# Kernel optimization log

Measured on AMD Instinct MI355X. Metric: run time of the kernel, lower is better.

Reference implementation:

```python
import jax, jax.numpy as jnp
import numpy as np
from jax.scipy.special import i0

# ---- NFFT configuration (matches init_kwargs) ----
N = (256, 256)          # output spectral size
n = (512, 512)          # oversampled grid size (sigma = 2)
M_PTS = 262144          # nonequispaced points
MWIN = 4                # window cutoff m
SIGMA = 2.0             # n[i]/N[i]
B_KB = (2.0 - 1.0 / SIGMA) * np.pi  # Kaiser-Bessel shape parameter

_n_arr = jnp.asarray(n, dtype=jnp.float32)


def _phi(k):
    """Kaiser-Bessel window, k: (..., d) -> (...,). Matches KaiserBesselWindow.forward."""
    arg = jnp.sqrt(MWIN ** 2 - (_n_arr * k) ** 2)
    out = jnp.sinh(B_KB * arg) / (arg * jnp.pi)
    out = jnp.nan_to_num(out, nan=0.0)
    return jnp.prod(out, axis=-1)


def _phi_hat():
    """Fourier coefficients of the window on the N-grid, shape (N1, N2)."""
    axes = [jnp.arange(-N[i] // 2, N[i] // 2, dtype=jnp.float32) for i in range(2)]
    grid = jnp.stack(jnp.meshgrid(*axes, indexing='ij'), axis=-1)  # (N1, N2, 2)
    ft = i0(MWIN * jnp.sqrt(B_KB ** 2 - (2.0 * jnp.pi * grid / _n_arr) ** 2))
    return jnp.prod(ft, axis=-1)


def setup_inputs() -> dict:
    key = jax.random.key(0)
    k1, k2, k3 = jax.random.split(key, 3)
    x = jax.random.uniform(k1, (1, 1, M_PTS, 2), dtype=jnp.float32,
                           minval=-0.5, maxval=0.5)
    f_hat_real = jax.random.normal(k2, (1, 1, N[0], N[1]), dtype=jnp.float32)
    f_hat_imag = jax.random.normal(k3, (1, 1, N[0], N[1]), dtype=jnp.float32)
    return {"x": x, "f_hat_real": f_hat_real, "f_hat_imag": f_hat_imag}


def _forward_nfft(x, f_hat):
    B, C = f_hat.shape[0], f_hat.shape[1]
    phi_hat = _phi_hat().astype(f_hat.real.dtype)
    # deconvolution + zero-padding to the oversampled grid
    g_hat = f_hat / phi_hat
    pad0 = (n[0] - N[0]) // 2
    pad1 = (n[1] - N[1]) // 2
    g_hat = jnp.pad(g_hat, ((0, 0), (0, 0), (pad0, pad0), (pad1, pad1)))
    # FFT (norm='backward': unnormalized forward transform)
    g_hat = jnp.fft.fftshift(g_hat, axes=(-2, -1))
    g = jnp.fft.fft2(g_hat)
    g = jnp.fft.ifftshift(g, axes=(-2, -1))  # (B, C, n1, n2)

    # ---- sparse (windowed) convolution: gather per point ----
    w = jnp.arange(2 * MWIN, dtype=jnp.int32)
    window = jnp.stack(jnp.meshgrid(w, w, indexing='ij'), axis=-1)
    window = window.reshape(-1, 1, 1, 1, 2)                    # (W,1,1,1,2)
    base = jnp.ceil(x * _n_arr).astype(jnp.int32) - MWIN        # (B,1,M,2)
    inds = base[None] + window                                  # (W,B,1,M,2)
    increments = _phi(x[None] - inds.astype(jnp.float32) / _n_arr)  # (W,B,1,M)
    n_i = jnp.asarray(n, dtype=jnp.int32)
    im = (inds + n_i // 2) % n_i                                # wrap to grid
    lin = im[..., 0] * n[1] + im[..., 1]                        # (W,B,1,M)
    lin = (lin
           + (n[0] * n[1]) * jnp.arange(C, dtype=jnp.int32).reshape(1, 1, C, 1)
           + (n[0] * n[1] * C) * jnp.arange(B, dtype=jnp.int32).reshape(1, B, 1, 1))
    g_l = g.reshape(-1)[lin]                                    # (W,B,C,M) gather
    f = jnp.sum(g_l * increments.astype(g.dtype), axis=0)       # (B,C,M)
    return f


def reference(x, f_hat_real, f_hat_imag):
    f_hat = (f_hat_real + 1j * f_hat_imag).astype(jnp.complex64)
    return _forward_nfft(x, f_hat)
```

## Files before the change

kernel.cpp:

```cpp
#include <hip/hip_runtime.h>
#include <math.h>

#define NPTS 262144
#define B_KB 4.71238898038469f
#define B_KB2 22.2066099025f
#define PI_F 3.14159265358979f
#define INV_2PI 0.15915494309f
#define TWO_PI_OVER_N 0.01227184630309f
#define NCOL 520
#define S_SCALE 1.37438953472e11f
#define INV_S   7.27595761418e-12f

typedef _Float16 half8v __attribute__((ext_vector_type(8)));
typedef _Float16 half4v __attribute__((ext_vector_type(4)));

__device__ __forceinline__ float i0f_dev(float x) {
    float ax = fabsf(x);
    if (ax < 3.75f) {
        float t = ax / 3.75f; t *= t;
        return 1.0f + t*(3.5156229f + t*(3.0899424f + t*(1.2067492f +
               t*(0.2659732f + t*(0.0360768f + t*0.0045813f)))));
    } else {
        float t = 3.75f / ax;
        float p = 0.39894228f + t*(0.01328592f + t*(0.00225319f + t*(-0.00157565f +
                  t*(0.00916281f + t*(-0.02057706f + t*(0.02635537f +
                  t*(-0.01647633f + t*0.00392377f)))))));
        return expf(ax) * p / sqrtf(ax);
    }
}

__device__ __forceinline__ float phi_win(float t) {
    float s = 16.0f - t * t;
    if (s <= 0.0f) return 0.0f;
    float a = sqrtf(s);
    float ez = __expf(B_KB * a);
    return (ez - __builtin_amdgcn_rcpf(ez)) * INV_2PI * __builtin_amdgcn_rcpf(a);
}

__global__ void rowfft_build(const float* __restrict__ fr,
                             const float* __restrict__ fi,
                             float2* __restrict__ g) {
    __shared__ float2 buf[512];
    int r = blockIdx.x;
    int i1 = (r < 128) ? r : r + 256;
    int k1 = (r < 128) ? r : r - 256;
    int tid = threadIdx.x;
    float a1 = TWO_PI_OVER_N * (float)k1;
    float ph1 = i0f_dev(4.0f * sqrtf(B_KB2 - a1 * a1));

    int k2 = tid - 128;
    int i2 = k2 & 511;
    float a2 = TWO_PI_OVER_N * (float)k2;
    float ph2 = i0f_dev(4.0f * sqrtf(B_KB2 - a2 * a2));
    float inv = S_SCALE / (ph1 * ph2);
    if ((i1 + i2) & 1) inv = -inv;
    int fidx = (k1 + 128) * 256 + (k2 + 128);
    float2 v = make_float2(fr[fidx] * inv, fi[fidx] * inv);

    buf[tid] = make_float2(0.0f, 0.0f);
    buf[tid + 256] = make_float2(0.0f, 0.0f);
    __syncthreads();
    int ri = (int)(__brev((unsigned)i2) >> 23);
    buf[ri] = v;
    __syncthreads();

    #pragma unroll
    for (int s = 1; s <= 9; ++s) {
        int half = 1 << (s - 1);
        int pos = tid & (half - 1);
        int j1 = ((tid >> (s - 1)) << s) | pos;
        float ang = -PI_F * (float)pos / (float)half;
        float sw, cw;
        __sincosf(ang, &sw, &cw);
        float2 u = buf[j1];
        float2 w = buf[j1 + half];
        float wr = cw * w.x - sw * w.y;
        float wi = cw * w.y + sw * w.x;
        buf[j1]        = make_float2(u.x + wr, u.y + wi);
        buf[j1 + half] = make_float2(u.x - wr, u.y - wi);
        __syncthreads();
    }
    long base = (long)i1 * NCOL;
    for (int j = tid; j < 512; j += 256) g[base + j] = buf[j];
    if (tid < 8) g[base + 512 + tid] = buf[tid];
}

__global__ void colfft_real(const float2* __restrict__ g,
                            float* __restrict__ gre) {
    __shared__ float2 buf[512];
    int c = blockIdx.x;
    int tid = threadIdx.x;
    buf[tid] = make_float2(0.0f, 0.0f);
    buf[tid + 256] = make_float2(0.0f, 0.0f);
    __syncthreads();
    int r = (tid < 128) ? tid : tid + 256;
    int rr = (int)(__brev((unsigned)r) >> 23);
    buf[rr] = g[(long)r * NCOL + c];
    __syncthreads();
    #pragma unroll
    for (int s = 1; s <= 9; ++s) {
        int half = 1 << (s - 1);
        int pos = tid & (half - 1);
        int j1 = ((tid >> (s - 1)) << s) | pos;
        float ang = -PI_F * (float)pos / (float)half;
        float sw, cw;
        __sincosf(ang, &sw, &cw);
        float2 u = buf[j1];
        float2 w = buf[j1 + half];
        float wr = cw * w.x - sw * w.y;
        float wi = cw * w.y + sw * w.x;
        buf[j1]        = make_float2(u.x + wr, u.y + wi);
        buf[j1 + half] = make_float2(u.x - wr, u.y - wi);
        __syncthreads();
    }
    for (int j = tid; j < 512; j += 256) gre[(long)j * NCOL + c] = buf[j].x;
}

__global__ void build_quads(const float* __restrict__ gre,
                            _Float16* __restrict__ qg) {
    int u = blockIdx.x;
    int s = u >> 7, rq = u & 127;
    int tid = threadIdx.x;
    int r0 = 4 * rq + s;
    const float* g0 = gre + (long)((r0    ) & 511) * NCOL;
    const float* g1 = gre + (long)((r0 + 1) & 511) * NCOL;
    const float* g2 = gre + (long)((r0 + 2) & 511) * NCOL;
    const float* g3 = gre + (long)((r0 + 3) & 511) * NCOL;
    _Float16* outb = qg + ((long)u * NCOL << 2);
    for (int c = tid; c < NCOL; c += 256) {
        half4v w;
        w[0] = (_Float16)g0[c];
        w[1] = (_Float16)g1[c];
        w[2] = (_Float16)g2[c];
        w[3] = (_Float16)g3[c];
        *reinterpret_cast<half4v*>(outb + ((long)c << 2)) = w;
    }
}

__global__ __launch_bounds__(256)
void gather_quads(const float2* __restrict__ x,
                  const _Float16* __restrict__ qg,
                  float* __restrict__ out) {
    int t = blockIdx.x * 256 + threadIdx.x;
    int m = t >> 1;
    int h = t & 1;
    float2 xv = x[m];
    float v1 = xv.x * 512.0f;
    float v2 = xv.y * 512.0f;
    float c1 = ceilf(v1), c2 = ceilf(v2);
    int b1 = (int)c1 - 4, b2 = (int)c2 - 4;
    float f1 = c1 - v1, f2 = c2 - v2;

    float phi2[8];
    #pragma unroll
    for (int j = 0; j < 8; ++j) phi2[j] = phi_win(4.0f - (float)j - f2);
    float phi1h[4];
    #pragma unroll
    for (int r = 0; r < 4; ++r)
        phi1h[r] = phi_win(4.0f - (float)(4 * h + r) - f1);

    int b1p = (b1 + 768) & 511;
    int b2p = (b2 + 768) & 511;
    int s  = b1p & 3;
    int rq = ((b1p >> 2) + h) & 127;
    const _Float16* base = qg + (((long)(s * 128 + rq) * NCOL + b2p) << 2);

    half8v rv[4];
    #pragma unroll
    for (int li = 0; li < 4; ++li)
        rv[li] = *reinterpret_cast<const half8v*>(base + (li << 3));

    float acc = 0.0f;
    #pragma unroll
    for (int li = 0; li < 4; ++li) {
        #pragma unroll
        for (int k = 0; k < 8; ++k) {
            int j = (li << 1) + (k >> 2);
            int r = k & 3;
            acc += (float)rv[li][k] * (phi1h[r] * phi2[j]);
        }
    }
    acc += __shfl_xor(acc, 1);
    if (h == 0) out[m] = acc * INV_S;
}

__global__ void build_ghat(const float* __restrict__ fr,
                           const float* __restrict__ fi,
                           float2* __restrict__ g, int ldg) {
    int idx = blockIdx.x * 256 + threadIdx.x;
    int i1 = idx >> 9;
    int i2 = idx & 511;
    float2 val = make_float2(0.0f, 0.0f);
    int k1 = 0, k2 = 0;
    bool ok = true;
    if (i1 < 128) k1 = i1; else if (i1 >= 384) k1 = i1 - 512; else ok = false;
    if (ok) { if (i2 < 128) k2 = i2; else if (i2 >= 384) k2 = i2 - 512; else ok = false; }
    if (ok) {
        float a1 = TWO_PI_OVER_N * (float)k1;
        float a2 = TWO_PI_OVER_N * (float)k2;
        float ph1 = i0f_dev(4.0f * sqrtf(B_KB2 - a1*a1));
        float ph2 = i0f_dev(4.0f * sqrtf(B_KB2 - a2*a2));
        float inv = 1.0f / (ph1 * ph2);
        if ((i1 + i2) & 1) inv = -inv;
        int fidx = (k1 + 128) * 256 + (k2 + 128);
        val.x = fr[fidx] * inv;
        val.y = fi[fidx] * inv;
    }
    g[i1 * ldg + i2] = val;
}

__global__ void fft_lines(float2* __restrict__ g, int line_stride,
                          int elem_stride, int ndup) {
    __shared__ float2 buf[512];
    int line = blockIdx.x;
    int tid = threadIdx.x;
    long base = (long)line * line_stride;
    for (int j = tid; j < 512; j += 256) {
        int rj = (int)(__brev((unsigned)j) >> 23);
        buf[rj] = g[base + (long)j * elem_stride];
    }
    __syncthreads();
    #pragma unroll
    for (int s = 1; s <= 9; ++s) {
        int half = 1 << (s - 1);
        int pos = tid & (half - 1);
        int i1 = ((tid >> (s - 1)) << s) | pos;
        float ang = -PI_F * (float)pos / (float)half;
        float sw, cw;
        __sincosf(ang, &sw, &cw);
        float2 u = buf[i1];
        float2 v = buf[i1 + half];
        float wr = cw * v.x - sw * v.y;
        float wi = cw * v.y + sw * v.x;
        buf[i1]        = make_float2(u.x + wr, u.y + wi);
        buf[i1 + half] = make_float2(u.x - wr, u.y - wi);
        __syncthreads();
    }
    for (int j = tid; j < 512; j += 256) g[base + (long)j * elem_stride] = buf[j];
    for (int j = tid; j < ndup; j += 256) g[base + 512 + j] = buf[j];
}

template<int COMPLEX>
__global__ __launch_bounds__(256, 4)
void gather_pad(const float2* __restrict__ x,
                const float2* __restrict__ g,
                float* __restrict__ out) {
    int m = blockIdx.x * 256 + threadIdx.x;
    float2 xv = x[m];
    float v1 = xv.x * 512.0f;
    float v2 = xv.y * 512.0f;
    float c1 = ceilf(v1), c2 = ceilf(v2);
    int b1 = (int)c1 - 4, b2 = (int)c2 - 4;
    float f1 = c1 - v1, f2 = c2 - v2;

    float phi1[8], phi2[8];
    int rowb[8];
    #pragma unroll
    for (int w = 0; w < 8; ++w) {
        phi1[w] = phi_win(4.0f - (float)w - f1);
        phi2[w] = phi_win(4.0f - (float)w - f2);
        rowb[w] = ((b1 + w + 768) & 511) * NCOL;
    }
    int cb = (b2 + 768) & 511;

    float accx = 0.0f, accy = 0.0f;
    #pragma unroll
    for (int w1 = 0; w1 < 8; ++w1) {
        const float4* p = reinterpret_cast<const float4*>(g + rowb[w1] + cb);
        float4 va = p[0], vb = p[1], vc = p[2], vd = p[3];
        float p1 = phi1[w1];
        accx += p1 * (phi2[0]*va.x + phi2[1]*va.z + phi2[2]*vb.x + phi2[3]*vb.z +
                      phi2[4]*vc.x + phi2[5]*vc.z + phi2[6]*vd.x + phi2[7]*vd.z);
        if (COMPLEX)
            accy += p1 * (phi2[0]*va.y + phi2[1]*va.w + phi2[2]*vb.y + phi2[3]*vb.w +
                          phi2[4]*vc.y + phi2[5]*vc.w + phi2[6]*vd.y + phi2[7]*vd.w);
    }
    if (COMPLEX) ((float2*)out)[m] = make_float2(accx, accy);
    else out[m] = accx;
}

extern "C" void kernel_launch(void* const* d_in, const int* in_sizes, int n_in,
                              void* d_out, int out_size, void* d_ws, size_t ws_size,
                              hipStream_t stream) {
    const float* x  = (const float*)d_in[0];
    const float* fr = (const float*)d_in[1];
    const float* fi = (const float*)d_in[2];
    int cplx = (out_size >= 2 * NPTS) ? 1 : 0;

    size_t g_bytes   = (size_t)512 * NCOL * sizeof(float2);
    size_t gre_bytes = (size_t)512 * NCOL * sizeof(float);
    size_t qg_bytes  = (size_t)512 * NCOL * 4 * sizeof(_Float16);
    char* ws = (char*)d_ws;
    float2*   g   = (float2*)ws;
    float*    gre = (float*)(ws + g_bytes);
    _Float16* qg  = (_Float16*)(ws + g_bytes + gre_bytes);
    size_t need = g_bytes + gre_bytes + qg_bytes;

    if (!cplx && ws_size >= need) {
        rowfft_build<<<256, 256, 0, stream>>>(fr, fi, g);
        colfft_real<<<NCOL, 256, 0, stream>>>(g, gre);
        build_quads<<<512, 256, 0, stream>>>(gre, qg);
        gather_quads<<<2048, 256, 0, stream>>>((const float2*)x, qg, (float*)d_out);
    } else if (ws_size >= g_bytes) {
        build_ghat<<<1024, 256, 0, stream>>>(fr, fi, g, NCOL);
        fft_lines<<<512, 256, 0, stream>>>(g, NCOL, 1, 8);
        fft_lines<<<NCOL, 256, 0, stream>>>(g, 1, NCOL, 0);
        if (cplx)
            gather_pad<1><<<1024, 256, 0, stream>>>((const float2*)x, g, (float*)d_out);
        else
            gather_pad<0><<<1024, 256, 0, stream>>>((const float2*)x, g, (float*)d_out);
    } else {
        build_ghat<<<1024, 256, 0, stream>>>(fr, fi, g, 512);
        fft_lines<<<512, 256, 0, stream>>>(g, 512, 1, 0);
        fft_lines<<<512, 256, 0, stream>>>(g, 1, 512, 0);
        if (cplx)
            gather_pad<1><<<1024, 256, 0, stream>>>((const float2*)x, g, (float*)d_out);
        else
            gather_pad<0><<<1024, 256, 0, stream>>>((const float2*)x, g, (float*)d_out);
    }
}
```

Before: 28.25 us.

## Pack eight grid rows per fp16 vector so each point reads one contiguous segment

```diff
diff --git a/kernel.cpp b/kernel.cpp
--- a/kernel.cpp
+++ b/kernel.cpp
@@ -12,7 +12,6 @@
 #define INV_S   7.27595761418e-12f
 
 typedef _Float16 half8v __attribute__((ext_vector_type(8)));
-typedef _Float16 half4v __attribute__((ext_vector_type(4)));
 
 __device__ __forceinline__ float i0f_dev(float x) {
     float ax = fabsf(x);
@@ -116,31 +115,35 @@
     for (int j = tid; j < 512; j += 256) gre[(long)j * NCOL + c] = buf[j].x;
 }
 
-__global__ void build_quads(const float* __restrict__ gre,
-                            _Float16* __restrict__ qg) {
+__global__ void build_octs(const float* __restrict__ gre,
+                           _Float16* __restrict__ og) {
     int u = blockIdx.x;
-    int s = u >> 7, rq = u & 127;
+    int s = u >> 6, ro = u & 63;
     int tid = threadIdx.x;
-    int r0 = 4 * rq + s;
-    const float* g0 = gre + (long)((r0    ) & 511) * NCOL;
-    const float* g1 = gre + (long)((r0 + 1) & 511) * NCOL;
-    const float* g2 = gre + (long)((r0 + 2) & 511) * NCOL;
-    const float* g3 = gre + (long)((r0 + 3) & 511) * NCOL;
-    _Float16* outb = qg + ((long)u * NCOL << 2);
+    int r0 = 8 * ro + s;
+    const float* gp0 = gre + (long)((r0    ) & 511) * NCOL;
+    const float* gp1 = gre + (long)((r0 + 1) & 511) * NCOL;
+    const float* gp2 = gre + (long)((r0 + 2) & 511) * NCOL;
+    const float* gp3 = gre + (long)((r0 + 3) & 511) * NCOL;
+    const float* gp4 = gre + (long)((r0 + 4) & 511) * NCOL;
+    const float* gp5 = gre + (long)((r0 + 5) & 511) * NCOL;
+    const float* gp6 = gre + (long)((r0 + 6) & 511) * NCOL;
+    const float* gp7 = gre + (long)((r0 + 7) & 511) * NCOL;
+    _Float16* outb = og + ((long)u * NCOL << 3);
     for (int c = tid; c < NCOL; c += 256) {
-        half4v w;
-        w[0] = (_Float16)g0[c];
-        w[1] = (_Float16)g1[c];
-        w[2] = (_Float16)g2[c];
-        w[3] = (_Float16)g3[c];
-        *reinterpret_cast<half4v*>(outb + ((long)c << 2)) = w;
+        half8v w;
+        w[0] = (_Float16)gp0[c]; w[1] = (_Float16)gp1[c];
+        w[2] = (_Float16)gp2[c]; w[3] = (_Float16)gp3[c];
+        w[4] = (_Float16)gp4[c]; w[5] = (_Float16)gp5[c];
+        w[6] = (_Float16)gp6[c]; w[7] = (_Float16)gp7[c];
+        *reinterpret_cast<half8v*>(outb + ((long)c << 3)) = w;
     }
 }
 
 __global__ __launch_bounds__(256)
-void gather_quads(const float2* __restrict__ x,
-                  const _Float16* __restrict__ qg,
-                  float* __restrict__ out) {
+void gather_oct(const float2* __restrict__ x,
+                const _Float16* __restrict__ og,
+                float* __restrict__ out) {
     int t = blockIdx.x * 256 + threadIdx.x;
     int m = t >> 1;
     int h = t & 1;
@@ -151,34 +154,28 @@
     int b1 = (int)c1 - 4, b2 = (int)c2 - 4;
     float f1 = c1 - v1, f2 = c2 - v2;
 
-    float phi2[8];
-    #pragma unroll
-    for (int j = 0; j < 8; ++j) phi2[j] = phi_win(4.0f - (float)j - f2);
-    float phi1h[4];
-    #pragma unroll
-    for (int r = 0; r < 4; ++r)
-        phi1h[r] = phi_win(4.0f - (float)(4 * h + r) - f1);
-
     int b1p = (b1 + 768) & 511;
     int b2p = (b2 + 768) & 511;
-    int s  = b1p & 3;
-    int rq = ((b1p >> 2) + h) & 127;
-    const _Float16* base = qg + (((long)(s * 128 + rq) * NCOL + b2p) << 2);
+    int s  = b1p & 7;
+    int ro = b1p >> 3;
+    const _Float16* seg = og + (((long)(s * 64 + ro) * NCOL + b2p) << 3);
 
     half8v rv[4];
     #pragma unroll
-    for (int li = 0; li < 4; ++li)
-        rv[li] = *reinterpret_cast<const half8v*>(base + (li << 3));
-
+    for (int i = 0; i < 4; ++i)
+        rv[i] = *reinterpret_cast<const half8v*>(seg + (((i << 1) | h) << 3));
+
+    float phi1[8];
+    #pragma unroll
+    for (int r = 0; r < 8; ++r) phi1[r] = phi_win(4.0f - (float)r - f1);
     float acc = 0.0f;
     #pragma unroll
-    for (int li = 0; li < 4; ++li) {
+    for (int i = 0; i < 4; ++i) {
+        float p2 = phi_win(4.0f - (float)((i << 1) | h) - f2);
+        float rs = 0.0f;
         #pragma unroll
-        for (int k = 0; k < 8; ++k) {
-            int j = (li << 1) + (k >> 2);
-            int r = k & 3;
-            acc += (float)rv[li][k] * (phi1h[r] * phi2[j]);
-        }
+        for (int r = 0; r < 8; ++r) rs += (float)rv[i][r] * phi1[r];
+        acc += p2 * rs;
     }
     acc += __shfl_xor(acc, 1);
     if (h == 0) out[m] = acc * INV_S;
@@ -289,18 +286,18 @@
 
     size_t g_bytes   = (size_t)512 * NCOL * sizeof(float2);
     size_t gre_bytes = (size_t)512 * NCOL * sizeof(float);
-    size_t qg_bytes  = (size_t)512 * NCOL * 4 * sizeof(_Float16);
+    size_t og_bytes  = (size_t)512 * NCOL * 8 * sizeof(_Float16);
     char* ws = (char*)d_ws;
     float2*   g   = (float2*)ws;
     float*    gre = (float*)(ws + g_bytes);
-    _Float16* qg  = (_Float16*)(ws + g_bytes + gre_bytes);
-    size_t need = g_bytes + gre_bytes + qg_bytes;
+    _Float16* og  = (_Float16*)(ws + g_bytes + gre_bytes);
+    size_t need = g_bytes + gre_bytes + og_bytes;
 
     if (!cplx && ws_size >= need) {
         rowfft_build<<<256, 256, 0, stream>>>(fr, fi, g);
         colfft_real<<<NCOL, 256, 0, stream>>>(g, gre);
-        build_quads<<<512, 256, 0, stream>>>(gre, qg);
-        gather_quads<<<2048, 256, 0, stream>>>((const float2*)x, qg, (float*)d_out);
+        build_octs<<<512, 256, 0, stream>>>(gre, og);
+        gather_oct<<<2048, 256, 0, stream>>>((const float2*)x, og, (float*)d_out);
     } else if (ws_size >= g_bytes) {
         build_ghat<<<1024, 256, 0, stream>>>(fr, fi, g, NCOL);
         fft_lines<<<512, 256, 0, stream>>>(g, NCOL, 1, 8);
```

Measured after the change: 30.99 us. 1.1x slower.

## Fuse column FFT with fp16 quad-grid build; split phi evaluation across lane pair

Applied to the files above, without the earlier changes.

```diff
diff --git a/kernel.cpp b/kernel.cpp
--- a/kernel.cpp
+++ b/kernel.cpp
@@ -85,8 +85,8 @@
     if (tid < 8) g[base + 512 + tid] = buf[tid];
 }
 
-__global__ void colfft_real(const float2* __restrict__ g,
-                            float* __restrict__ gre) {
+__global__ void colfft_quads(const float2* __restrict__ g,
+                             _Float16* __restrict__ qg) {
     __shared__ float2 buf[512];
     int c = blockIdx.x;
     int tid = threadIdx.x;
@@ -113,27 +113,18 @@
         buf[j1 + half] = make_float2(u.x - wr, u.y - wi);
         __syncthreads();
     }
-    for (int j = tid; j < 512; j += 256) gre[(long)j * NCOL + c] = buf[j].x;
-}
-
-__global__ void build_quads(const float* __restrict__ gre,
-                            _Float16* __restrict__ qg) {
-    int u = blockIdx.x;
-    int s = u >> 7, rq = u & 127;
-    int tid = threadIdx.x;
-    int r0 = 4 * rq + s;
-    const float* g0 = gre + (long)((r0    ) & 511) * NCOL;
-    const float* g1 = gre + (long)((r0 + 1) & 511) * NCOL;
-    const float* g2 = gre + (long)((r0 + 2) & 511) * NCOL;
-    const float* g3 = gre + (long)((r0 + 3) & 511) * NCOL;
-    _Float16* outb = qg + ((long)u * NCOL << 2);
-    for (int c = tid; c < NCOL; c += 256) {
+    #pragma unroll
+    for (int u0 = 0; u0 < 2; ++u0) {
+        int u = tid + u0 * 256;
+        int rq = u & 127;
+        int s = u >> 7;
+        int r0 = 4 * rq + s;
         half4v w;
-        w[0] = (_Float16)g0[c];
-        w[1] = (_Float16)g1[c];
-        w[2] = (_Float16)g2[c];
-        w[3] = (_Float16)g3[c];
-        *reinterpret_cast<half4v*>(outb + ((long)c << 2)) = w;
+        w[0] = (_Float16)buf[(r0    ) & 511].x;
+        w[1] = (_Float16)buf[(r0 + 1) & 511].x;
+        w[2] = (_Float16)buf[(r0 + 2) & 511].x;
+        w[3] = (_Float16)buf[(r0 + 3) & 511].x;
+        *reinterpret_cast<half4v*>(qg + (((long)u * NCOL + c) << 2)) = w;
     }
 }
 
@@ -151,14 +142,6 @@
     int b1 = (int)c1 - 4, b2 = (int)c2 - 4;
     float f1 = c1 - v1, f2 = c2 - v2;
 
-    float phi2[8];
-    #pragma unroll
-    for (int j = 0; j < 8; ++j) phi2[j] = phi_win(4.0f - (float)j - f2);
-    float phi1h[4];
-    #pragma unroll
-    for (int r = 0; r < 4; ++r)
-        phi1h[r] = phi_win(4.0f - (float)(4 * h + r) - f1);
-
     int b1p = (b1 + 768) & 511;
     int b2p = (b2 + 768) & 511;
     int s  = b1p & 3;
@@ -170,6 +153,23 @@
     for (int li = 0; li < 4; ++li)
         rv[li] = *reinterpret_cast<const half8v*>(base + (li << 3));
 
+    float phi1h[4];
+    #pragma unroll
+    for (int r = 0; r < 4; ++r)
+        phi1h[r] = phi_win(4.0f - (float)(4 * h + r) - f1);
+    float p2own[4], p2oth[4];
+    #pragma unroll
+    for (int r = 0; r < 4; ++r) {
+        p2own[r] = phi_win(4.0f - (float)(4 * h + r) - f2);
+        p2oth[r] = __shfl_xor(p2own[r], 1);
+    }
+    float ph2[8];
+    #pragma unroll
+    for (int j = 0; j < 8; ++j) {
+        float a = p2own[j & 3], b = p2oth[j & 3];
+        ph2[j] = ((j >> 2) == h) ? a : b;
+    }
+
     float acc = 0.0f;
     #pragma unroll
     for (int li = 0; li < 4; ++li) {
@@ -177,7 +177,7 @@
         for (int k = 0; k < 8; ++k) {
             int j = (li << 1) + (k >> 2);
             int r = k & 3;
-            acc += (float)rv[li][k] * (phi1h[r] * phi2[j]);
+            acc += (float)rv[li][k] * (phi1h[r] * ph2[j]);
         }
     }
     acc += __shfl_xor(acc, 1);
@@ -287,19 +287,16 @@
     const float* fi = (const float*)d_in[2];
     int cplx = (out_size >= 2 * NPTS) ? 1 : 0;
 
-    size_t g_bytes   = (size_t)512 * NCOL * sizeof(float2);
-    size_t gre_bytes = (size_t)512 * NCOL * sizeof(float);
-    size_t qg_bytes  = (size_t)512 * NCOL * 4 * sizeof(_Float16);
+    size_t g_bytes  = (size_t)512 * NCOL * sizeof(float2);
+    size_t qg_bytes = (size_t)512 * NCOL * 4 * sizeof(_Float16);
     char* ws = (char*)d_ws;
-    float2*   g   = (float2*)ws;
-    float*    gre = (float*)(ws + g_bytes);
-    _Float16* qg  = (_Float16*)(ws + g_bytes + gre_bytes);
-    size_t need = g_bytes + gre_bytes + qg_bytes;
+    float2*   g  = (float2*)ws;
+    _Float16* qg = (_Float16*)(ws + g_bytes);
+    size_t need = g_bytes + qg_bytes;
 
     if (!cplx && ws_size >= need) {
         rowfft_build<<<256, 256, 0, stream>>>(fr, fi, g);
-        colfft_real<<<NCOL, 256, 0, stream>>>(g, gre);
-        build_quads<<<512, 256, 0, stream>>>(gre, qg);
+        colfft_quads<<<NCOL, 256, 0, stream>>>(g, qg);
         gather_quads<<<2048, 256, 0, stream>>>((const float2*)x, qg, (float*)d_out);
     } else if (ws_size >= g_bytes) {
         build_ghat<<<1024, 256, 0, stream>>>(fr, fi, g, NCOL);
```

After: 26.22 us. 1.08x faster.
